# Kernel optimization log

Hardware: AMD Instinct MI355X
Metric: run time of the kernel (lower is better)

Reference implementation:

```python
import jax, jax.numpy as jnp
import numpy as np

L = 8        # n_blocks
D = 768      # embed_dim
NH = 12      # num_heads
HD = D // NH # head_dim = 64
SG = 16      # scene_grid_size -> 256 scene tokens
GG = 7       # glimpse_grid_size -> 49 local tokens
GATE_INIT = 0.1
B = 64
SCALE = 1.0 / np.sqrt(HD)


def grid_positions(G):
    # cell-center coordinates in [0,1], row-major, (x, y) order -> [G*G, 2]
    c = (jnp.arange(G, dtype=jnp.float32) + 0.5) / G
    yy, xx = jnp.meshgrid(c, c, indexing='ij')
    return jnp.stack([xx.ravel(), yy.ravel()], axis=-1)


def compute_rope(pos, periods):
    # pos: [B, N, 2], periods: [HD//4] -> cos/sin each [B, N, HD//2]
    ang = (2.0 * jnp.pi) * pos[..., None] / periods  # [B, N, 2, HD//4]
    ang = ang.reshape(pos.shape[0], pos.shape[1], -1)
    return jnp.cos(ang), jnp.sin(ang)


def apply_rope(x, cos, sin):
    # x: [B, H, N, HD]; cos/sin: [B, N, HD//2]
    c = cos[:, None]
    s = sin[:, None]
    x1, x2 = jnp.split(x, 2, axis=-1)
    return jnp.concatenate([x1 * c - x2 * s, x1 * s + x2 * c], axis=-1)


def layer_norm(x, w, b):
    m = jnp.mean(x, axis=-1, keepdims=True)
    v = jnp.var(x, axis=-1, keepdims=True)
    return (x - m) * jax.lax.rsqrt(v + 1e-6) * w + b


def heads(x, n):  # [B, N, D] -> [B, H, N, HD]
    b = x.shape[0]
    return x.reshape(b, n, NH, HD).transpose(0, 2, 1, 3)


def merge(x, n):  # [B, H, N, HD] -> [B, N, D]
    return x.transpose(0, 2, 1, 3).reshape(x.shape[0], n, D)


def cross_attn(x, ctx, Wq, bq, Wk, bk, Wv, bv, Wo, bo, q_rope, kv_rope):
    n, m = x.shape[1], ctx.shape[1]
    q = apply_rope(heads(x @ Wq + bq, n), *q_rope)
    k = apply_rope(heads(ctx @ Wk + bk, m), *kv_rope)
    v = heads(ctx @ Wv + bv, m)
    a = jax.nn.softmax(jnp.einsum('bhnd,bhmd->bhnm', q, k) * SCALE, axis=-1)
    o = merge(jnp.einsum('bhnm,bhmd->bhnd', a, v), n)
    return o @ Wo + bo


def backend_block(x, rope, ln1w, ln1b, Wqkv, bqkv, Wp, bp, ln2w, ln2b, W1, b1, W2, b2):
    n = x.shape[1]
    h = layer_norm(x, ln1w, ln1b)
    q, k, v = jnp.split(h @ Wqkv + bqkv, 3, axis=-1)
    q = apply_rope(heads(q, n), *rope)
    k = apply_rope(heads(k, n), *rope)
    v = heads(v, n)
    a = jax.nn.softmax(jnp.einsum('bhnd,bhmd->bhnm', q, k) * SCALE, axis=-1)
    x = x + merge(jnp.einsum('bhnm,bhmd->bhnd', a, v), n) @ Wp + bp
    h = layer_norm(x, ln2w, ln2b)
    return x + jax.nn.gelu(h @ W1 + b1, approximate=False) @ W2 + b2


def setup_inputs() -> dict:
    key = jax.random.key(0)
    ks = iter(jax.random.split(key, 64))

    def nrm(shape, s=0.02):
        return jax.random.normal(next(ks), shape, dtype=jnp.float32) * s

    inp = {
        'local': jax.random.normal(next(ks), (B, GG * GG, D), dtype=jnp.float32),
        'centers': jax.random.uniform(next(ks), (B, 2), dtype=jnp.float32),
        'scales': jax.random.uniform(next(ks), (B, 2), dtype=jnp.float32),
        'scene_tokens': nrm((1, SG * SG, D)),
        'periods': (10.0 ** jnp.linspace(-2.0, 0.0, HD // 4)).astype(jnp.float32),
        'read_gate': jnp.full((L, D), GATE_INIT, jnp.float32),
        'write_gate': jnp.full((L, D), GATE_INIT, jnp.float32),
        'ln1_w': jnp.ones((L, D), jnp.float32), 'ln1_b': jnp.zeros((L, D), jnp.float32),
        'ln2_w': jnp.ones((L, D), jnp.float32), 'ln2_b': jnp.zeros((L, D), jnp.float32),
        'Wqkv': nrm((L, D, 3 * D)), 'bqkv': jnp.zeros((L, 3 * D), jnp.float32),
        'Wp': nrm((L, D, D)), 'bp': jnp.zeros((L, D), jnp.float32),
        'W1': nrm((L, D, 4 * D)), 'b1': jnp.zeros((L, 4 * D), jnp.float32),
        'W2': nrm((L, 4 * D, D)), 'b2': jnp.zeros((L, D), jnp.float32),
    }
    for pre in ('r', 'w'):
        for nm in ('q', 'k', 'v', 'o'):
            inp[f'{pre}{nm}_W'] = nrm((L, D, D))
            inp[f'{pre}{nm}_b'] = jnp.zeros((L, D), jnp.float32)
    return inp


def reference(local, centers, scales, scene_tokens, periods,
              rq_W, rq_b, rk_W, rk_b, rv_W, rv_b, ro_W, ro_b,
              wq_W, wq_b, wk_W, wk_b, wv_W, wv_b, wo_W, wo_b,
              read_gate, write_gate,
              ln1_w, ln1_b, Wqkv, bqkv, Wp, bp, ln2_w, ln2_b, W1, b1, W2, b2):
    b = local.shape[0]
    scene = jnp.broadcast_to(scene_tokens, (b, SG * SG, D))
    # glimpse-derived per-token positions
    local_pos = centers[:, None, :] + scales[:, None, :] * (grid_positions(GG)[None] - 0.5)
    scene_pos = jnp.broadcast_to(grid_positions(SG)[None], (b, SG * SG, 2))
    local_rope = compute_rope(local_pos, periods)
    scene_rope = compute_rope(scene_pos, periods)
    for i in range(L):
        local = local + read_gate[i] * cross_attn(
            local, scene, rq_W[i], rq_b[i], rk_W[i], rk_b[i], rv_W[i], rv_b[i],
            ro_W[i], ro_b[i], local_rope, scene_rope)
        local = backend_block(local, local_rope, ln1_w[i], ln1_b[i], Wqkv[i], bqkv[i],
                              Wp[i], bp[i], ln2_w[i], ln2_b[i], W1[i], b1[i], W2[i], b2[i])
        scene = scene + write_gate[i] * cross_attn(
            scene, local, wq_W[i], wq_b[i], wk_W[i], wk_b[i], wv_W[i], wv_b[i],
            wo_W[i], wo_b[i], scene_rope, local_rope)
    return local, scene
```

## Files before the change

kernel.cpp:

```cpp
#include <hip/hip_runtime.h>
#include <hip/hip_bf16.h>
#include <math.h>

#define BATCH 64
#define DM 768
#define NHD 12
#define NLAYER 8
#define NLOC 49
#define NSC 256
#define ATT_SCALE 0.125f
#define ML (BATCH * NLOC)
#define ML_PAD 3200
#define MS (BATCH * NSC)

typedef short bf16x8 __attribute__((ext_vector_type(8)));
typedef float f32x4 __attribute__((ext_vector_type(4)));

__device__ __forceinline__ float bf2f(unsigned short r) {
  return __uint_as_float(((unsigned)r) << 16);
}
__device__ __forceinline__ unsigned short f2bf(float x) {
  __hip_bfloat16 h = __float2bfloat16(x);
  unsigned short r;
  __builtin_memcpy(&r, &h, 2);
  return r;
}

__global__ void rope_local_k(const float* __restrict__ centers, const float* __restrict__ scales,
                             const float* __restrict__ periods, float* __restrict__ lcos,
                             float* __restrict__ lsin) {
  int t = blockIdx.x * blockDim.x + threadIdx.x;
  const int total = BATCH * NLOC * 32;
  if (t >= total) return;
  int d = t & 31;
  int r = (t >> 5) % NLOC;
  int b = t / (NLOC * 32);
  int pi = d & 15;
  float gx = ((r % 7) + 0.5f) / 7.0f - 0.5f;
  float gy = ((r / 7) + 0.5f) / 7.0f - 0.5f;
  float coord = (d < 16) ? (centers[b * 2 + 0] + scales[b * 2 + 0] * gx)
                         : (centers[b * 2 + 1] + scales[b * 2 + 1] * gy);
  float ang = 6.283185307179586f * coord / periods[pi];
  lcos[t] = cosf(ang);
  lsin[t] = sinf(ang);
}

__global__ void rope_scene_k(const float* __restrict__ periods, float* __restrict__ scos,
                             float* __restrict__ ssin) {
  int t = blockIdx.x * blockDim.x + threadIdx.x;
  const int total = NSC * 32;
  if (t >= total) return;
  int d = t & 31;
  int r = t >> 5;
  int pi = d & 15;
  float coord = (d < 16) ? ((r % 16) + 0.5f) / 16.0f : ((r / 16) + 0.5f) / 16.0f;
  float ang = 6.283185307179586f * coord / periods[pi];
  scos[t] = cosf(ang);
  ssin[t] = sinf(ang);
}

__global__ void init_out_k(const float* __restrict__ local_in, const float* __restrict__ scene_tok,
                           float* __restrict__ out, unsigned short* __restrict__ lbf,
                           unsigned short* __restrict__ sbf) {
  int t = blockIdx.x * blockDim.x + threadIdx.x;
  const int NL = ML * DM;
  const int NS = MS * DM;
  if (t < NL) {
    float v = local_in[t];
    out[t] = v;
    lbf[t] = f2bf(v);
  } else if (t < NL + NS) {
    float v = scene_tok[(t - NL) % (NSC * DM)];
    out[t] = v;
    sbf[t - NL] = f2bf(v);
  }
}

__global__ void pad_zero_k(unsigned short* __restrict__ bq, unsigned short* __restrict__ bk,
                           unsigned short* __restrict__ bv) {
  int t = blockIdx.x * blockDim.x + threadIdx.x;
  if (t < 64 * 2304) bq[(size_t)ML * 2304 + t] = 0;
  if (t < 64 * 768) {
    bk[(size_t)ML * 768 + t] = 0;
    bv[(size_t)ML * 768 + t] = 0;
  }
}

struct SrcPtrs {
  const float* p[12];
};

__constant__ const int wc_K[12] = {768, 768, 768, 3072, 768, 768, 768, 768, 768, 768, 768, 768};
__constant__ const int wc_N[12] = {2304, 768, 3072, 768, 768, 768, 768, 768, 768, 768, 768, 768};
__constant__ const int wc_blk[13] = {0,    1728, 2304, 4608, 6912,  7488,  8064,
                                     8640, 9216, 9792, 10368, 10944, 11520};
__constant__ const size_t wc_off[12] = {0,       1769472, 2359296, 4718592,
                                        7077888, 7667712, 8257536, 8847360,
                                        9437184, 10027008, 10616832, 11206656};
#define W_QKV 0
#define W_P 1769472
#define W_1 2359296
#define W_2 4718592
#define W_RQ 7077888
#define W_RK 7667712
#define W_RV 8257536
#define W_RO 8847360
#define W_WQ 9437184
#define W_WK 10027008
#define W_WV 10616832
#define W_WO 11206656

__global__ __launch_bounds__(256) void wconv_k(SrcPtrs sp, unsigned short* __restrict__ dst) {
  int b = blockIdx.x;
  int mi = 0;
  while (b >= wc_blk[mi + 1]) ++mi;
  int lb = b - wc_blk[mi];
  int K = wc_K[mi], N = wc_N[mi];
  int ncol = N >> 5;
  int kt = lb / ncol, nt = lb - kt * ncol;
  const float* src = sp.p[mi];
  __shared__ unsigned short tile[32][33];
  int r = threadIdx.x >> 3, c4 = (threadIdx.x & 7) << 2;
  float4 v = *(const float4*)(src + (size_t)(kt * 32 + r) * N + nt * 32 + c4);
  tile[r][c4 + 0] = f2bf(v.x);
  tile[r][c4 + 1] = f2bf(v.y);
  tile[r][c4 + 2] = f2bf(v.z);
  tile[r][c4 + 3] = f2bf(v.w);
  __syncthreads();
  unsigned short o[4];
  o[0] = tile[c4 + 0][r];
  o[1] = tile[c4 + 1][r];
  o[2] = tile[c4 + 2][r];
  o[3] = tile[c4 + 3][r];
  unsigned short* dp = dst + wc_off[mi] + (size_t)(nt * 32 + r) * K + kt * 32 + c4;
  *(ushort4*)dp = *(const ushort4*)o;
}

template <int MODE, int RMODE>
__global__ __launch_bounds__(256) void gemm_mfma(const unsigned short* __restrict__ A,
                                                 const unsigned short* __restrict__ Bt,
                                                 const float* __restrict__ bias,
                                                 unsigned short* __restrict__ Cb,
                                                 float* __restrict__ Cf,
                                                 const float* __restrict__ gate,
                                                 const float* __restrict__ rc,
                                                 const float* __restrict__ rsn, int ropemax,
                                                 int M, int N, int K) {
  __shared__ unsigned short As[128 * 64];
  __shared__ unsigned short Bs[128 * 64];
  const int tid = threadIdx.x;
  const int w = tid >> 6;
  const int lane = tid & 63;
  const int wm = w & 1, wn = w >> 1;
  const int bm = blockIdx.y << 7;
  const int bn = blockIdx.x << 7;
  const int lrow = lane >> 3;
  const int lchunk = lane & 7;
  const int schunk = lchunk ^ lrow;
  const int fm = lane & 15;
  const int quad = lane >> 4;

  f32x4 acc[4][4];
#pragma unroll
  for (int i = 0; i < 4; ++i)
#pragma unroll
    for (int j = 0; j < 4; ++j) acc[i][j] = (f32x4){0.f, 0.f, 0.f, 0.f};

  const size_t a_base = (size_t)(bm + w * 32 + lrow) * K + schunk * 8;
  const size_t b_base = (size_t)(bn + w * 32 + lrow) * K + schunk * 8;

  for (int k0 = 0; k0 < K; k0 += 64) {
    __syncthreads();
#pragma unroll
    for (int q = 0; q < 4; ++q) {
      const unsigned short* ga = A + a_base + (size_t)(q * 8) * K + k0;
      const unsigned short* gb = Bt + b_base + (size_t)(q * 8) * K + k0;
      __builtin_amdgcn_global_load_lds((const __attribute__((address_space(1))) void*)ga,
                                       (__attribute__((address_space(3))) void*)(As + (w * 32 + q * 8) * 64),
                                       16, 0, 0);
      __builtin_amdgcn_global_load_lds((const __attribute__((address_space(1))) void*)gb,
                                       (__attribute__((address_space(3))) void*)(Bs + (w * 32 + q * 8) * 64),
                                       16, 0, 0);
    }
    __syncthreads();
#pragma unroll
    for (int kc = 0; kc < 2; ++kc) {
      bf16x8 af[4], bfr[4];
#pragma unroll
      for (int i = 0; i < 4; ++i) {
        int ra = wm * 64 + i * 16 + fm;
        af[i] = *(const bf16x8*)(As + ra * 64 + (((kc * 4 + quad) ^ (ra & 7)) << 3));
      }
#pragma unroll
      for (int j = 0; j < 4; ++j) {
        int rb = wn * 64 + j * 16 + fm;
        bfr[j] = *(const bf16x8*)(Bs + rb * 64 + (((kc * 4 + quad) ^ (rb & 7)) << 3));
      }
#pragma unroll
      for (int i = 0; i < 4; ++i)
#pragma unroll
        for (int j = 0; j < 4; ++j)
          acc[i][j] = __builtin_amdgcn_mfma_f32_16x16x32_bf16(af[i], bfr[j], acc[i][j], 0, 0, 0);
    }
  }

  if constexpr (RMODE > 0) {
#pragma unroll
    for (int jp = 0; jp < 2; ++jp) {
      const int colA = bn + wn * 64 + jp * 16 + fm;
      const int colB = colA + 32;
      const float bA = bias[colA];
      const float bB = bias[colB];
      const bool doRope = (colA < ropemax);
      const int ddv = (jp << 4) + fm;
#pragma unroll
      for (int i = 0; i < 4; ++i) {
#pragma unroll
        for (int reg = 0; reg < 4; ++reg) {
          const int row = bm + wm * 64 + i * 16 + quad * 4 + reg;
          if (row < M) {
            float x1 = acc[i][jp][reg] + bA;
            float x2 = acc[i][jp + 2][reg] + bB;
            if (doRope) {
              const int ti = (RMODE == 1) ? row : (row & 255);
              const float c = rc[ti * 32 + ddv];
              const float s = rsn[ti * 32 + ddv];
              const float y1 = x1 * c - x2 * s;
              x2 = x1 * s + x2 * c;
              x1 = y1;
            }
            const size_t base = (size_t)row * N;
            Cb[base + colA] = f2bf(x1);
            Cb[base + colB] = f2bf(x2);
          }
        }
      }
    }
  } else {
#pragma unroll
    for (int j = 0; j < 4; ++j) {
      const int col = bn + wn * 64 + j * 16 + fm;
      const float bj = bias[col];
      float gj = 1.0f;
      if (MODE == 2) gj = gate ? gate[col] : 1.0f;
#pragma unroll
      for (int i = 0; i < 4; ++i) {
#pragma unroll
        for (int reg = 0; reg < 4; ++reg) {
          const int row = bm + wm * 64 + i * 16 + quad * 4 + reg;
          if (row < M) {
            float v = acc[i][j][reg] + bj;
            if (MODE == 1) v = 0.5f * v * (1.0f + erff(v * 0.7071067811865475f));
            const size_t idx = (size_t)row * N + col;
            if (MODE == 2) {
              float o = Cf[idx] + gj * v;
              Cf[idx] = o;
              Cb[idx] = f2bf(o);
            } else {
              Cb[idx] = f2bf(v);
            }
          }
        }
      }
    }
  }
}

__global__ __launch_bounds__(256) void ln_k(const float* __restrict__ X,
                                            const float* __restrict__ w,
                                            const float* __restrict__ bb,
                                            unsigned short* __restrict__ Y, int rows) {
  const int wid = threadIdx.x >> 6, lane = threadIdx.x & 63;
  const int row = blockIdx.x * 4 + wid;
  if (row >= rows) return;
  const float* x = X + (size_t)row * DM;
  float v[12];
  float s = 0.f;
#pragma unroll
  for (int j = 0; j < 12; ++j) {
    v[j] = x[lane + 64 * j];
    s += v[j];
  }
#pragma unroll
  for (int o = 32; o; o >>= 1) s += __shfl_xor(s, o, 64);
  float mean = s * (1.0f / 768.0f);
  float q = 0.f;
#pragma unroll
  for (int j = 0; j < 12; ++j) {
    float d0 = v[j] - mean;
    q += d0 * d0;
  }
#pragma unroll
  for (int o = 32; o; o >>= 1) q += __shfl_xor(q, o, 64);
  float inv = rsqrtf(q * (1.0f / 768.0f) + 1e-6f);
#pragma unroll
  for (int j = 0; j < 12; ++j) {
    int d0 = lane + 64 * j;
    Y[(size_t)row * DM + d0] = f2bf((v[j] - mean) * inv * w[d0] + bb[d0]);
  }
}

__global__ __launch_bounds__(256) void attn_k(const unsigned short* __restrict__ Q, int qs,
                                              const unsigned short* __restrict__ K, int ks,
                                              const unsigned short* __restrict__ V, int vs,
                                              unsigned short* __restrict__ O, int Nq, int Nk) {
  __shared__ unsigned short q_s[32 * 64];
  __shared__ unsigned short k_s[64 * 64];
  __shared__ unsigned short v_s[64 * 64];
  __shared__ __align__(16) float sc[32][68];
  __shared__ float m_s[32], l_s[32], rs_s[32];

  const int tid = threadIdx.x;
  const int nQT = (Nq + 31) >> 5;
  const int qt = blockIdx.x % nQT;
  const int h = (blockIdx.x / nQT) % NHD;
  const int b = blockIdx.x / (nQT * NHD);
  const int n0 = qt << 5;
  const int nrows = (Nq - n0 < 32) ? (Nq - n0) : 32;

  const int w = tid >> 6;
  const int lane = tid & 63;
  const int fm = lane & 15;
  const int quad = lane >> 4;
  const int lrow = lane >> 3;
  const int lchunk = lane & 7;
  const int schunk = lchunk ^ lrow;

  if (tid < 32) {
    m_s[tid] = -1e30f;
    l_s[tid] = 0.f;
  }

  {
    const unsigned short* gq =
        Q + ((size_t)b * Nq + n0 + w * 8 + lrow) * qs + h * 64 + schunk * 8;
    __builtin_amdgcn_global_load_lds((const __attribute__((address_space(1))) void*)gq,
                                     (__attribute__((address_space(3))) void*)(q_s + w * 8 * 64),
                                     16, 0, 0);
  }

  float acc[8] = {0.f, 0.f, 0.f, 0.f, 0.f, 0.f, 0.f, 0.f};

  for (int m0 = 0; m0 < Nk; m0 += 64) {
    const int mc = (Nk - m0 < 64) ? (Nk - m0) : 64;
    __syncthreads();
#pragma unroll
    for (int g = 0; g < 2; ++g) {
      const int rg = w * 16 + g * 8;
      const size_t grow = (size_t)b * Nk + m0 + rg + lrow;
      const unsigned short* gk = K + grow * ks + h * 64 + schunk * 8;
      const unsigned short* gv = V + grow * vs + h * 64 + lchunk * 8;
      __builtin_amdgcn_global_load_lds((const __attribute__((address_space(1))) void*)gk,
                                       (__attribute__((address_space(3))) void*)(k_s + rg * 64),
                                       16, 0, 0);
      __builtin_amdgcn_global_load_lds((const __attribute__((address_space(1))) void*)gv,
                                       (__attribute__((address_space(3))) void*)(v_s + rg * 64),
                                       16, 0, 0);
    }
    __syncthreads();

    {
      const int rt = w & 1;
      const int arow = (rt << 4) + fm;
      const bf16x8 a0 = *(const bf16x8*)(q_s + (arow << 6) + ((quad ^ (arow & 7)) << 3));
      const bf16x8 a1 = *(const bf16x8*)(q_s + (arow << 6) + (((4 + quad) ^ (arow & 7)) << 3));
      const int ct0 = (w >> 1) << 1;
#pragma unroll
      for (int j = 0; j < 2; ++j) {
        const int brow = ((ct0 + j) << 4) + fm;
        const bf16x8 b0 = *(const bf16x8*)(k_s + (brow << 6) + ((quad ^ (brow & 7)) << 3));
        const bf16x8 b1 = *(const bf16x8*)(k_s + (brow << 6) + (((4 + quad) ^ (brow & 7)) << 3));
        f32x4 sv = (f32x4){0.f, 0.f, 0.f, 0.f};
        sv = __builtin_amdgcn_mfma_f32_16x16x32_bf16(a0, b0, sv, 0, 0, 0);
        sv = __builtin_amdgcn_mfma_f32_16x16x32_bf16(a1, b1, sv, 0, 0, 0);
        const int srow = (rt << 4) + (quad << 2);
        const int scol = ((ct0 + j) << 4) + fm;
#pragma unroll
        for (int reg = 0; reg < 4; ++reg) sc[srow + reg][scol] = sv[reg] * ATT_SCALE;
      }
    }
    __syncthreads();

    {
      const int r = (w << 3) + lrow;
      const int c0 = lchunk << 3;
      float4 pa = *(const float4*)&sc[r][c0];
      float4 pb = *(const float4*)&sc[r][c0 + 4];
      float vv[8] = {pa.x, pa.y, pa.z, pa.w, pb.x, pb.y, pb.z, pb.w};
      float mx = -1e30f;
#pragma unroll
      for (int e = 0; e < 8; ++e) {
        if (c0 + e >= mc) vv[e] = -1e30f;
        mx = fmaxf(mx, vv[e]);
      }
      mx = fmaxf(mx, __shfl_xor(mx, 1, 64));
      mx = fmaxf(mx, __shfl_xor(mx, 2, 64));
      mx = fmaxf(mx, __shfl_xor(mx, 4, 64));
      const float mo = m_s[r];
      const float mn = fmaxf(mo, mx);
      float sum = 0.f;
#pragma unroll
      for (int e = 0; e < 8; ++e) {
        const float ev = (c0 + e < mc) ? __expf(vv[e] - mn) : 0.f;
        vv[e] = ev;
        sum += ev;
      }
      *(float4*)&sc[r][c0] = (float4){vv[0], vv[1], vv[2], vv[3]};
      *(float4*)&sc[r][c0 + 4] = (float4){vv[4], vv[5], vv[6], vv[7]};
      sum += __shfl_xor(sum, 1, 64);
      sum += __shfl_xor(sum, 2, 64);
      sum += __shfl_xor(sum, 4, 64);
      if (lchunk == 0) {
        const float sca = __expf(mo - mn);
        rs_s[r] = sca;
        l_s[r] = l_s[r] * sca + sum;
        m_s[r] = mn;
      }
    }
    __syncthreads();

#pragma unroll
    for (int rr = 0; rr < 8; ++rr) acc[rr] *= rs_s[w + (rr << 2)];
#pragma unroll 4
    for (int m = 0; m < 64; m += 4) {
      float4 p[8];
#pragma unroll
      for (int rr = 0; rr < 8; ++rr) p[rr] = *(const float4*)&sc[w + (rr << 2)][m];
      const float v0 = bf2f(v_s[(m + 0) * 64 + lane]);
      const float v1 = bf2f(v_s[(m + 1) * 64 + lane]);
      const float v2 = bf2f(v_s[(m + 2) * 64 + lane]);
      const float v3 = bf2f(v_s[(m + 3) * 64 + lane]);
#pragma unroll
      for (int rr = 0; rr < 8; ++rr) {
        acc[rr] = fmaf(p[rr].x, v0, acc[rr]);
        acc[rr] = fmaf(p[rr].y, v1, acc[rr]);
        acc[rr] = fmaf(p[rr].z, v2, acc[rr]);
        acc[rr] = fmaf(p[rr].w, v3, acc[rr]);
      }
    }
  }

#pragma unroll
  for (int rr = 0; rr < 8; ++rr) {
    const int r = w + (rr << 2);
    if (r < nrows)
      O[((size_t)b * Nq + n0 + r) * DM + h * 64 + lane] = f2bf(acc[rr] / l_s[r]);
  }
}

extern "C" void kernel_launch(void* const* d_in, const int* in_sizes, int n_in, void* d_out,
                              int out_size, void* d_ws, size_t ws_size, hipStream_t stream) {
  const float* local_in = (const float*)d_in[0];
  const float* centers = (const float*)d_in[1];
  const float* scales = (const float*)d_in[2];
  const float* scene_tok = (const float*)d_in[3];
  const float* periods = (const float*)d_in[4];
  const float* read_gate = (const float*)d_in[5];
  const float* write_gate = (const float*)d_in[6];
  const float* ln1w = (const float*)d_in[7];
  const float* ln1b = (const float*)d_in[8];
  const float* ln2w = (const float*)d_in[9];
  const float* ln2b = (const float*)d_in[10];
  const float* Wqkv = (const float*)d_in[11];
  const float* bqkv = (const float*)d_in[12];
  const float* Wp = (const float*)d_in[13];
  const float* bp = (const float*)d_in[14];
  const float* W1 = (const float*)d_in[15];
  const float* b1 = (const float*)d_in[16];
  const float* W2 = (const float*)d_in[17];
  const float* b2 = (const float*)d_in[18];
  const float* rqW = (const float*)d_in[19];
  const float* rqb = (const float*)d_in[20];
  const float* rkW = (const float*)d_in[21];
  const float* rkb = (const float*)d_in[22];
  const float* rvW = (const float*)d_in[23];
  const float* rvb = (const float*)d_in[24];
  const float* roW = (const float*)d_in[25];
  const float* rob = (const float*)d_in[26];
  const float* wqW = (const float*)d_in[27];
  const float* wqb = (const float*)d_in[28];
  const float* wkW = (const float*)d_in[29];
  const float* wkb = (const float*)d_in[30];
  const float* wvW = (const float*)d_in[31];
  const float* wvb = (const float*)d_in[32];
  const float* woW = (const float*)d_in[33];
  const float* wob = (const float*)d_in[34];

  float* out = (float*)d_out;
  float* local = out;
  float* scene = out + (size_t)ML * DM;

  constexpr size_t E_WSLOT = 11796480;
  constexpr size_t E_LBF = (size_t)ML_PAD * DM;
  constexpr size_t E_BUF = (size_t)MS * DM;
  unsigned short* wslot = (unsigned short*)d_ws;
  unsigned short* local_bf = wslot + E_WSLOT;
  unsigned short* scene_bf = local_bf + E_LBF;
  unsigned short* bufQ = scene_bf + E_BUF;
  unsigned short* bufK = bufQ + E_BUF;
  unsigned short* bufV = bufK + E_BUF;
  unsigned short* bufO = bufV + E_BUF;
  unsigned short* bufH = bufO + E_BUF;
  float* lcos = (float*)(bufH + E_LBF);
  float* lsin = lcos + BATCH * NLOC * 32;
  float* scos = lsin + BATCH * NLOC * 32;
  float* ssin = scos + NSC * 32;

  const int totOut = (ML + MS) * DM;
  init_out_k<<<(totOut + 255) / 256, 256, 0, stream>>>(local_in, scene_tok, out, local_bf,
                                                       scene_bf);
  pad_zero_k<<<(64 * 2304 + 255) / 256, 256, 0, stream>>>(bufQ, bufK, bufV);
  rope_local_k<<<(BATCH * NLOC * 32 + 255) / 256, 256, 0, stream>>>(centers, scales, periods,
                                                                    lcos, lsin);
  rope_scene_k<<<(NSC * 32 + 255) / 256, 256, 0, stream>>>(periods, scos, ssin);

  const size_t DD = (size_t)DM * DM;
  const dim3 gS(6, MS / 128);
  const dim3 gL(6, ML_PAD / 128);
  for (int i = 0; i < NLAYER; ++i) {
    SrcPtrs sp;
    sp.p[0] = Wqkv + (size_t)DM * 3 * DM * i;
    sp.p[1] = Wp + DD * i;
    sp.p[2] = W1 + (size_t)DM * 4 * DM * i;
    sp.p[3] = W2 + (size_t)4 * DM * DM * i;
    sp.p[4] = rqW + DD * i;
    sp.p[5] = rkW + DD * i;
    sp.p[6] = rvW + DD * i;
    sp.p[7] = roW + DD * i;
    sp.p[8] = wqW + DD * i;
    sp.p[9] = wkW + DD * i;
    sp.p[10] = wvW + DD * i;
    sp.p[11] = woW + DD * i;
    wconv_k<<<11520, 256, 0, stream>>>(sp, wslot);

    gemm_mfma<0, 1><<<gL, 256, 0, stream>>>(local_bf, wslot + W_RQ, rqb + DM * i, bufQ, nullptr,
                                            nullptr, lcos, lsin, DM, ML, DM, DM);
    gemm_mfma<0, 2><<<gS, 256, 0, stream>>>(scene_bf, wslot + W_RK, rkb + DM * i, bufK, nullptr,
                                            nullptr, scos, ssin, DM, MS, DM, DM);
    gemm_mfma<0, 0><<<gS, 256, 0, stream>>>(scene_bf, wslot + W_RV, rvb + DM * i, bufV, nullptr,
                                            nullptr, nullptr, nullptr, 0, MS, DM, DM);
    attn_k<<<dim3(BATCH * NHD * 2), 256, 0, stream>>>(bufQ, DM, bufK, DM, bufV, DM, bufO, NLOC,
                                                      NSC);
    gemm_mfma<2, 0><<<gL, 256, 0, stream>>>(bufO, wslot + W_RO, rob + DM * i, local_bf, local,
                                            read_gate + DM * i, nullptr, nullptr, 0, ML, DM, DM);
    ln_k<<<ML / 4, 256, 0, stream>>>(local, ln1w + DM * i, ln1b + DM * i, bufH, ML);
    gemm_mfma<0, 1><<<dim3(18, ML_PAD / 128), 256, 0, stream>>>(bufH, wslot + W_QKV,
                                                                bqkv + 3 * DM * i, bufQ, nullptr,
                                                                nullptr, lcos, lsin, 2 * DM, ML,
                                                                3 * DM, DM);
    attn_k<<<dim3(BATCH * NHD * 2), 256, 0, stream>>>(bufQ, 3 * DM, bufQ + DM, 3 * DM,
                                                      bufQ + 2 * DM, 3 * DM, bufO, NLOC, NLOC);
    gemm_mfma<2, 0><<<gL, 256, 0, stream>>>(bufO, wslot + W_P, bp + DM * i, local_bf, local,
                                            nullptr, nullptr, nullptr, 0, ML, DM, DM);
    ln_k<<<ML / 4, 256, 0, stream>>>(local, ln2w + DM * i, ln2b + DM * i, bufH, ML);
    gemm_mfma<1, 0><<<dim3(24, ML_PAD / 128), 256, 0, stream>>>(bufH, wslot + W_1,
                                                                b1 + 4 * DM * i, bufO, nullptr,
                                                                nullptr, nullptr, nullptr, 0, ML,
                                                                4 * DM, DM);
    gemm_mfma<2, 0><<<gL, 256, 0, stream>>>(bufO, wslot + W_2, b2 + DM * i, local_bf, local,
                                            nullptr, nullptr, nullptr, 0, ML, DM, 4 * DM);
    gemm_mfma<0, 2><<<gS, 256, 0, stream>>>(scene_bf, wslot + W_WQ, wqb + DM * i, bufQ, nullptr,
                                            nullptr, scos, ssin, DM, MS, DM, DM);
    gemm_mfma<0, 1><<<gL, 256, 0, stream>>>(local_bf, wslot + W_WK, wkb + DM * i, bufK, nullptr,
                                            nullptr, lcos, lsin, DM, ML, DM, DM);
    gemm_mfma<0, 0><<<gL, 256, 0, stream>>>(local_bf, wslot + W_WV, wvb + DM * i, bufV, nullptr,
                                            nullptr, nullptr, nullptr, 0, ML, DM, DM);
    attn_k<<<dim3(BATCH * NHD * 8), 256, 0, stream>>>(bufQ, DM, bufK, DM, bufV, DM, bufO, NSC,
                                                      NLOC);
    gemm_mfma<2, 0><<<gS, 256, 0, stream>>>(bufO, wslot + W_WO, wob + DM * i, scene_bf, scene,
                                            write_gate + DM * i, nullptr, nullptr, 0, MS, DM, DM);
  }
}
```

Before: 5.489 ms.

## Fuse K and V projections into one GEMM and add XCD-aware block remap

The separate K and V projection GEMMs of both cross-attentions are merged into one GEMM with N=1536, writing an interleaved KV buffer. A second bias pointer covers the V half, and RoPE is limited to the K columns. Padding rows are now zeroed inside the GEMM epilogue, which removes the pad_zero kernel. Workgroup indices are also remapped so that consecutive tiles land on the same XCD for better L2 locality. Together these cut launches and A-operand rereads, at the cost of extra epilogue branching and the assumption that the wrk/wv weight slots sit next to each other.

```diff
diff --git a/kernel.cpp b/kernel.cpp
--- a/kernel.cpp
+++ b/kernel.cpp
@@ -73,16 +73,6 @@
     float v = scene_tok[(t - NL) % (NSC * DM)];
     out[t] = v;
     sbf[t - NL] = f2bf(v);
-  }
-}
-
-__global__ void pad_zero_k(unsigned short* __restrict__ bq, unsigned short* __restrict__ bk,
-                           unsigned short* __restrict__ bv) {
-  int t = blockIdx.x * blockDim.x + threadIdx.x;
-  if (t < 64 * 2304) bq[(size_t)ML * 2304 + t] = 0;
-  if (t < 64 * 768) {
-    bk[(size_t)ML * 768 + t] = 0;
-    bv[(size_t)ML * 768 + t] = 0;
   }
 }
 
@@ -140,20 +130,34 @@
 __global__ __launch_bounds__(256) void gemm_mfma(const unsigned short* __restrict__ A,
                                                  const unsigned short* __restrict__ Bt,
                                                  const float* __restrict__ bias,
+                                                 const float* __restrict__ bias2,
                                                  unsigned short* __restrict__ Cb,
                                                  float* __restrict__ Cf,
                                                  const float* __restrict__ gate,
                                                  const float* __restrict__ rc,
                                                  const float* __restrict__ rsn, int ropemax,
-                                                 int M, int N, int K) {
+                                                 int M, int Mpad, int N, int K) {
   __shared__ unsigned short As[128 * 64];
   __shared__ unsigned short Bs[128 * 64];
   const int tid = threadIdx.x;
   const int w = tid >> 6;
   const int lane = tid & 63;
   const int wm = w & 1, wn = w >> 1;
-  const int bm = blockIdx.y << 7;
-  const int bn = blockIdx.x << 7;
+
+  int bx, by;
+  {
+    const int gx = gridDim.x;
+    const int nwg = gx * gridDim.y;
+    const int lin = blockIdx.x + blockIdx.y * gx;
+    const int q = nwg >> 3, r = nwg & 7;
+    const int xcd = lin & 7, pos = lin >> 3;
+    const int nl = xcd * q + (xcd < r ? xcd : r) + pos;
+    bx = nl % gx;
+    by = nl / gx;
+  }
+  const int bm = by << 7;
+  const int bn = bx << 7;
+
   const int lrow = lane >> 3;
   const int lchunk = lane & 7;
   const int schunk = lchunk ^ lrow;
@@ -209,8 +213,8 @@
     for (int jp = 0; jp < 2; ++jp) {
       const int colA = bn + wn * 64 + jp * 16 + fm;
       const int colB = colA + 32;
-      const float bA = bias[colA];
-      const float bB = bias[colB];
+      const float bA = (bias2 && colA >= 768) ? bias2[colA - 768] : bias[colA];
+      const float bB = (bias2 && colA >= 768) ? bias2[colB - 768] : bias[colB];
       const bool doRope = (colA < ropemax);
       const int ddv = (jp << 4) + fm;
 #pragma unroll
@@ -232,6 +236,10 @@
             const size_t base = (size_t)row * N;
             Cb[base + colA] = f2bf(x1);
             Cb[base + colB] = f2bf(x2);
+          } else if (row < Mpad) {
+            const size_t base = (size_t)row * N;
+            Cb[base + colA] = 0;
+            Cb[base + colB] = 0;
           }
         }
       }
@@ -259,6 +267,8 @@
             } else {
               Cb[idx] = f2bf(v);
             }
+          } else if (row < Mpad && MODE == 0) {
+            Cb[(size_t)row * N + col] = 0;
           }
         }
       }
@@ -497,9 +507,8 @@
   unsigned short* local_bf = wslot + E_WSLOT;
   unsigned short* scene_bf = local_bf + E_LBF;
   unsigned short* bufQ = scene_bf + E_BUF;
-  unsigned short* bufK = bufQ + E_BUF;
-  unsigned short* bufV = bufK + E_BUF;
-  unsigned short* bufO = bufV + E_BUF;
+  unsigned short* bufKV = bufQ + E_BUF;
+  unsigned short* bufO = bufKV + 2 * E_BUF;
   unsigned short* bufH = bufO + E_BUF;
   float* lcos = (float*)(bufH + E_LBF);
   float* lsin = lcos + BATCH * NLOC * 32;
@@ -509,7 +518,6 @@
   const int totOut = (ML + MS) * DM;
   init_out_k<<<(totOut + 255) / 256, 256, 0, stream>>>(local_in, scene_tok, out, local_bf,
                                                        scene_bf);
-  pad_zero_k<<<(64 * 2304 + 255) / 256, 256, 0, stream>>>(bufQ, bufK, bufV);
   rope_local_k<<<(BATCH * NLOC * 32 + 255) / 256, 256, 0, stream>>>(centers, scales, periods,
                                                                     lcos, lsin);
   rope_scene_k<<<(NSC * 32 + 255) / 256, 256, 0, stream>>>(periods, scos, ssin);
@@ -517,6 +525,8 @@
   const size_t DD = (size_t)DM * DM;
   const dim3 gS(6, MS / 128);
   const dim3 gL(6, ML_PAD / 128);
+  const dim3 gSKV(12, MS / 128);
+  const dim3 gLKV(12, ML_PAD / 128);
   for (int i = 0; i < NLAYER; ++i) {
     SrcPtrs sp;
     sp.p[0] = Wqkv + (size_t)DM * 3 * DM * i;
@@ -533,41 +543,42 @@
     sp.p[11] = woW + DD * i;
     wconv_k<<<11520, 256, 0, stream>>>(sp, wslot);
 
-    gemm_mfma<0, 1><<<gL, 256, 0, stream>>>(local_bf, wslot + W_RQ, rqb + DM * i, bufQ, nullptr,
-                                            nullptr, lcos, lsin, DM, ML, DM, DM);
-    gemm_mfma<0, 2><<<gS, 256, 0, stream>>>(scene_bf, wslot + W_RK, rkb + DM * i, bufK, nullptr,
-                                            nullptr, scos, ssin, DM, MS, DM, DM);
-    gemm_mfma<0, 0><<<gS, 256, 0, stream>>>(scene_bf, wslot + W_RV, rvb + DM * i, bufV, nullptr,
-                                            nullptr, nullptr, nullptr, 0, MS, DM, DM);
-    attn_k<<<dim3(BATCH * NHD * 2), 256, 0, stream>>>(bufQ, DM, bufK, DM, bufV, DM, bufO, NLOC,
-                                                      NSC);
-    gemm_mfma<2, 0><<<gL, 256, 0, stream>>>(bufO, wslot + W_RO, rob + DM * i, local_bf, local,
-                                            read_gate + DM * i, nullptr, nullptr, 0, ML, DM, DM);
+    gemm_mfma<0, 1><<<gL, 256, 0, stream>>>(local_bf, wslot + W_RQ, rqb + DM * i, nullptr, bufQ,
+                                            nullptr, nullptr, lcos, lsin, DM, ML, ML_PAD, DM, DM);
+    gemm_mfma<0, 2><<<gSKV, 256, 0, stream>>>(scene_bf, wslot + W_RK, rkb + DM * i, rvb + DM * i,
+                                              bufKV, nullptr, nullptr, scos, ssin, DM, MS, MS,
+                                              2 * DM, DM);
+    attn_k<<<dim3(BATCH * NHD * 2), 256, 0, stream>>>(bufQ, DM, bufKV, 2 * DM, bufKV + DM,
+                                                      2 * DM, bufO, NLOC, NSC);
+    gemm_mfma<2, 0><<<gL, 256, 0, stream>>>(bufO, wslot + W_RO, rob + DM * i, nullptr, local_bf,
+                                            local, read_gate + DM * i, nullptr, nullptr, 0, ML,
+                                            ML, DM, DM);
     ln_k<<<ML / 4, 256, 0, stream>>>(local, ln1w + DM * i, ln1b + DM * i, bufH, ML);
     gemm_mfma<0, 1><<<dim3(18, ML_PAD / 128), 256, 0, stream>>>(bufH, wslot + W_QKV,
-                                                                bqkv + 3 * DM * i, bufQ, nullptr,
-                                                                nullptr, lcos, lsin, 2 * DM, ML,
-                                                                3 * DM, DM);
+                                                                bqkv + 3 * DM * i, nullptr, bufQ,
+                                                                nullptr, nullptr, lcos, lsin,
+                                                                2 * DM, ML, ML_PAD, 3 * DM, DM);
     attn_k<<<dim3(BATCH * NHD * 2), 256, 0, stream>>>(bufQ, 3 * DM, bufQ + DM, 3 * DM,
                                                       bufQ + 2 * DM, 3 * DM, bufO, NLOC, NLOC);
-    gemm_mfma<2, 0><<<gL, 256, 0, stream>>>(bufO, wslot + W_P, bp + DM * i, local_bf, local,
-                                            nullptr, nullptr, nullptr, 0, ML, DM, DM);
+    gemm_mfma<2, 0><<<gL, 256, 0, stream>>>(bufO, wslot + W_P, bp + DM * i, nullptr, local_bf,
+                                            local, nullptr, nullptr, nullptr, 0, ML, ML, DM, DM);
     ln_k<<<ML / 4, 256, 0, stream>>>(local, ln2w + DM * i, ln2b + DM * i, bufH, ML);
     gemm_mfma<1, 0><<<dim3(24, ML_PAD / 128), 256, 0, stream>>>(bufH, wslot + W_1,
-                                                                b1 + 4 * DM * i, bufO, nullptr,
-                                                                nullptr, nullptr, nullptr, 0, ML,
-                                                                4 * DM, DM);
-    gemm_mfma<2, 0><<<gL, 256, 0, stream>>>(bufO, wslot + W_2, b2 + DM * i, local_bf, local,
-                                            nullptr, nullptr, nullptr, 0, ML, DM, 4 * DM);
-    gemm_mfma<0, 2><<<gS, 256, 0, stream>>>(scene_bf, wslot + W_WQ, wqb + DM * i, bufQ, nullptr,
-                                            nullptr, scos, ssin, DM, MS, DM, DM);
-    gemm_mfma<0, 1><<<gL, 256, 0, stream>>>(local_bf, wslot + W_WK, wkb + DM * i, bufK, nullptr,
-                                            nullptr, lcos, lsin, DM, ML, DM, DM);
-    gemm_mfma<0, 0><<<gL, 256, 0, stream>>>(local_bf, wslot + W_WV, wvb + DM * i, bufV, nullptr,
-                                            nullptr, nullptr, nullptr, 0, ML, DM, DM);
-    attn_k<<<dim3(BATCH * NHD * 8), 256, 0, stream>>>(bufQ, DM, bufK, DM, bufV, DM, bufO, NSC,
-                                                      NLOC);
-    gemm_mfma<2, 0><<<gS, 256, 0, stream>>>(bufO, wslot + W_WO, wob + DM * i, scene_bf, scene,
-                                            write_gate + DM * i, nullptr, nullptr, 0, MS, DM, DM);
-  }
-}
+                                                                b1 + 4 * DM * i, nullptr, bufO,
+                                                                nullptr, nullptr, nullptr,
+                                                                nullptr, 0, ML, ML, 4 * DM, DM);
+    gemm_mfma<2, 0><<<gL, 256, 0, stream>>>(bufO, wslot + W_2, b2 + DM * i, nullptr, local_bf,
+                                            local, nullptr, nullptr, nullptr, 0, ML, ML, DM,
+                                            4 * DM);
+    gemm_mfma<0, 2><<<gS, 256, 0, stream>>>(scene_bf, wslot + W_WQ, wqb + DM * i, nullptr, bufQ,
+                                            nullptr, nullptr, scos, ssin, DM, MS, MS, DM, DM);
+    gemm_mfma<0, 1><<<gLKV, 256, 0, stream>>>(local_bf, wslot + W_WK, wkb + DM * i, wvb + DM * i,
+                                              bufKV, nullptr, nullptr, lcos, lsin, DM, ML,
+                                              ML_PAD, 2 * DM, DM);
+    attn_k<<<dim3(BATCH * NHD * 8), 256, 0, stream>>>(bufQ, DM, bufKV, 2 * DM, bufKV + DM,
+                                                      2 * DM, bufO, NSC, NLOC);
+    gemm_mfma<2, 0><<<gS, 256, 0, stream>>>(bufO, wslot + W_WO, wob + DM * i, nullptr, scene_bf,
+                                            scene, write_gate + DM * i, nullptr, nullptr, 0, MS,
+                                            MS, DM, DM);
+  }
+}
```

New measurement: 5.150 ms. -6.2%, faster.
